# Optimization experiments

Hardware: AMD Instinct MI355X
Metric: run time of the kernel (lower is better)

## Reference

```python
import jax, jax.numpy as jnp
import numpy as np

B, L, D, H, TOPK = 64, 1024, 16, 128, 64
SCALE = H ** -0.5  # proj_dim ** -0.5


def _linear_params(k, fan_in, fan_out):
    W = jax.random.normal(k, (fan_in, fan_out), jnp.float32) / np.sqrt(fan_in).astype(np.float32)
    b = jnp.zeros((fan_out,), jnp.float32)
    return W, b


def setup_inputs() -> dict:
    key = jax.random.key(0)
    ks = jax.random.split(key, 9)
    x = jax.random.normal(ks[0], (B, L, D), jnp.float32)
    Wq, bq = _linear_params(ks[1], D, H)
    Wk, bk = _linear_params(ks[2], D, H)
    phi_W1, phi_b1 = _linear_params(ks[3], D, H)
    phi_W2, phi_b2 = _linear_params(ks[4], H, H)
    xi_W1, xi_b1 = _linear_params(ks[5], 2 * D, H)
    xi_W2, xi_b2 = _linear_params(ks[6], H, H)
    rho_W1, rho_b1 = _linear_params(ks[7], H, H)
    rho_W2, rho_b2 = _linear_params(ks[8], H, H)
    return {
        "x": x,
        "Wq": Wq, "bq": bq, "Wk": Wk, "bk": bk,
        "phi_W1": phi_W1, "phi_b1": phi_b1, "phi_W2": phi_W2, "phi_b2": phi_b2,
        "xi_W1": xi_W1, "xi_b1": xi_b1, "xi_W2": xi_W2, "xi_b2": xi_b2,
        "rho_W1": rho_W1, "rho_b1": rho_b1, "rho_W2": rho_W2, "rho_b2": rho_b2,
    }


def _gather_rows(x, idx):
    # x: (B, L, D), idx: (B, K) -> (B, K, D)
    return jnp.take_along_axis(x, jnp.broadcast_to(idx[:, :, None], idx.shape + (x.shape[-1],)), axis=1)


def reference(x, Wq, bq, Wk, bk,
              phi_W1, phi_b1, phi_W2, phi_b2,
              xi_W1, xi_b1, xi_W2, xi_b2,
              rho_W1, rho_b1, rho_W2, rho_b2):
    # padding mask (trim is identity for dense random inputs; mask is all-True)
    mask = jnp.abs(x).sum(-1) != 0  # (B, L)
    Q = x @ Wq + bq                 # (B, L, H)
    K = x @ Wk + bk                 # (B, L, H)
    scores = jnp.einsum("blh,bmh->blm", Q, K) * SCALE  # (B, L, L)
    mask_2d = mask[:, :, None] & mask[:, None, :]
    scores = jnp.where(mask_2d, scores, -jnp.inf)
    flat = scores.reshape(B, L * L)
    topk_vals, topk_idx = jax.lax.top_k(flat, TOPK)    # (B, K)
    topk_w = jax.nn.softmax(topk_vals, axis=-1)
    row = topk_idx // L
    col = topk_idx % L
    x_i = _gather_rows(x, row)  # (B, K, D)
    x_j = _gather_rows(x, col)
    relu = jax.nn.relu
    feat_self = relu(x_i @ phi_W1 + phi_b1) @ phi_W2 + phi_b2
    pair = jnp.concatenate([x_i, x_j], axis=-1)
    feat_pair = relu(pair @ xi_W1 + xi_b1) @ xi_W2 + xi_b2
    self_mask = (row == col)[:, :, None]
    interaction = jnp.where(self_mask, feat_self, feat_pair)  # (B, K, H)
    pooled = jnp.sum(interaction * topk_w[:, :, None], axis=1)  # (B, H)
    return relu(pooled @ rho_W1 + rho_b1) @ rho_W2 + rho_b2
```

## Files before the change

### kernel.cpp

```cpp
#include <hip/hip_runtime.h>

typedef unsigned int uint;

#define SCALEF 0.08838834764831845f
#define NBINS 4096
#define CAND_MAX 4096
#define SELC 1024
#define LLIST 512
#define T_LOOSE 3.3f

__device__ __forceinline__ uint ordmap(float v) {
  uint u = __float_as_uint(v);
  return (u & 0x80000000u) ? ~u : (u | 0x80000000u);
}

#define DOT4(a, b2) ((a).x*(b2).x + (a).y*(b2).y + (a).z*(b2).z + (a).w*(b2).w)

__global__ __launch_bounds__(256) void k_prep(const float* __restrict__ x,
    const float* __restrict__ Wq, const float* __restrict__ bq,
    const float* __restrict__ Wk, const float* __restrict__ bk,
    float* __restrict__ Gv, float* __restrict__ Hv,
    uint* __restrict__ ghist, uint* __restrict__ ccnt, uint* __restrict__ ccnt2) {
  __shared__ float sWq[2048], sWk[2048];
  __shared__ float sA[256];
  __shared__ float su[16], sv[16], sc;
  int tid = threadIdx.x;
  int row = blockIdx.x * 256 + tid;
  ((uint4*)ghist)[row] = make_uint4(0u, 0u, 0u, 0u);
  if (blockIdx.x == 0 && tid < 128) { if (tid < 64) ccnt[tid] = 0; else ccnt2[tid - 64] = 0; }
  for (int i = tid; i < 512; i += 256) {
    ((float4*)sWq)[i] = ((const float4*)Wq)[i];
    ((float4*)sWk)[i] = ((const float4*)Wk)[i];
  }
  __syncthreads();
  {
    int d = tid >> 4, e = tid & 15;
    float s = 0.f;
#pragma unroll 8
    for (int h = 0; h < 128; h++) s += sWq[d * 128 + h] * sWk[e * 128 + h];
    sA[tid] = s * SCALEF;
  }
  if (tid < 16) {
    float s1 = 0.f, s2 = 0.f;
    for (int h = 0; h < 128; h++) { s1 += sWq[tid * 128 + h] * bk[h]; s2 += bq[h] * sWk[tid * 128 + h]; }
    su[tid] = s1 * SCALEF; sv[tid] = s2 * SCALEF;
  } else if (tid == 16) {
    float s = 0.f;
    for (int h = 0; h < 128; h++) s += bq[h] * bk[h];
    sc = s * SCALEF;
  }
  __syncthreads();
  float xr[16];
#pragma unroll
  for (int d = 0; d < 16; d += 4) *(float4*)&xr[d] = *(const float4*)&x[(size_t)row * 16 + d];
  float g[16];
#pragma unroll
  for (int e = 0; e < 16; e++) {
    float s = sv[e];
#pragma unroll
    for (int d = 0; d < 16; d++) s += xr[d] * sA[d * 16 + e];
    g[e] = s;
  }
  float hh = sc;
#pragma unroll
  for (int d = 0; d < 16; d++) hh += xr[d] * su[d];
#pragma unroll
  for (int e = 0; e < 16; e += 4) *(float4*)&Gv[(size_t)row * 16 + e] = *(float4*)&g[e];
  Hv[row] = hh;
}

template<int PHASE>
__global__ __launch_bounds__(256, 4) void k_score(const float* __restrict__ Gv,
    const float* __restrict__ Hv, const float* __restrict__ x,
    uint* __restrict__ ghist, uint* __restrict__ ccnt,
    int* __restrict__ cidx, float* __restrict__ cval,
    const float* __restrict__ tcut2, const uint* __restrict__ ccmain) {
  int i = blockIdx.x;
  int b = i >> 6, t = i & 63, tm = t >> 3, tn = t & 7;
  if (PHASE != 0) { uint c = ccmain[b]; if (c >= 64 && c <= CAND_MAX) return; }
  __shared__ float4 sX4[512];
  __shared__ int lidx[PHASE == 1 ? 1 : LLIST];
  __shared__ float lval[PHASE == 1 ? 1 : LLIST];
  __shared__ uint lcnt, base_sh;
  __shared__ uint shist[PHASE == 1 ? NBINS : 1];
  int tid = threadIdx.x;
  if (PHASE == 1)
    for (int s = tid; s < NBINS; s += 256) shist[s] = 0;
  if (tid == 0) lcnt = 0;
  const float4* xsrc = (const float4*)(x + ((size_t)b * 1024 + tn * 128) * 16);
  sX4[tid] = xsrc[tid];
  sX4[tid + 256] = xsrc[tid + 256];
  int lane = tid & 63, w = tid >> 6;
  const float4* gp = (const float4*)(Gv + ((size_t)b * 1024 + tm * 128 + lane) * 16);
  float4 gr0[4], gr1[4];
#pragma unroll
  for (int q = 0; q < 4; q++) { gr0[q] = gp[q]; gr1[q] = gp[256 + q]; }
  float h0 = Hv[b * 1024 + tm * 128 + lane];
  float h1v = Hv[b * 1024 + tm * 128 + lane + 64];
  float tc = (PHASE == 2) ? tcut2[b] : T_LOOSE;
  int r0g = tm * 128 + lane, c0g = tn * 128;
  __syncthreads();

#pragma unroll 4
  for (int cc = 0; cc < 32; ++cc) {
    int c = w * 32 + cc;
    float4 x0 = sX4[c * 4 + 0], x1 = sX4[c * 4 + 1];
    float4 x2 = sX4[c * 4 + 2], x3 = sX4[c * 4 + 3];
    float s0 = (h0 + DOT4(gr0[0], x0) + DOT4(gr0[1], x1)) + (DOT4(gr0[2], x2) + DOT4(gr0[3], x3));
    float s1 = (h1v + DOT4(gr1[0], x0) + DOT4(gr1[1], x1)) + (DOT4(gr1[2], x2) + DOT4(gr1[3], x3));
    if (PHASE == 1) {
      atomicAdd(&shist[ordmap(s0) >> 20], 1u);
      atomicAdd(&shist[ordmap(s1) >> 20], 1u);
    } else {
      if (s0 >= tc) {
        uint pos = atomicAdd(&lcnt, 1u);
        int fi = r0g * 1024 + (c0g + c);
        if (pos < LLIST) { lidx[pos] = fi; lval[pos] = s0; }
        else { uint gp2 = atomicAdd(&ccnt[b], 1u);
               if (gp2 < CAND_MAX) { cidx[b * CAND_MAX + gp2] = fi; cval[b * CAND_MAX + gp2] = s0; } }
      }
      if (s1 >= tc) {
        uint pos = atomicAdd(&lcnt, 1u);
        int fi = (r0g + 64) * 1024 + (c0g + c);
        if (pos < LLIST) { lidx[pos] = fi; lval[pos] = s1; }
        else { uint gp2 = atomicAdd(&ccnt[b], 1u);
               if (gp2 < CAND_MAX) { cidx[b * CAND_MAX + gp2] = fi; cval[b * CAND_MAX + gp2] = s1; } }
      }
    }
  }
  __syncthreads();
  if (PHASE == 1) {
    for (int s = tid; s < NBINS; s += 256) { uint cg = shist[s]; if (cg) atomicAdd(&ghist[b * NBINS + s], cg); }
  } else {
    uint n = lcnt > LLIST ? LLIST : lcnt;
    if (tid == 0) base_sh = atomicAdd(&ccnt[b], n);
    __syncthreads();
    for (uint j = tid; j < n; j += 256) {
      uint p = base_sh + j;
      if (p < CAND_MAX) { cidx[b * CAND_MAX + p] = lidx[j]; cval[b * CAND_MAX + p] = lval[j]; }
    }
  }
}

__global__ __launch_bounds__(256) void k_fb_thresh(const uint* __restrict__ ghist,
    const uint* __restrict__ ccmain, float* __restrict__ tcut2) {
  int b = blockIdx.x;
  { uint c = ccmain[b]; if (c >= 64 && c <= CAND_MAX) return; }
  int tid = threadIdx.x;
  __shared__ uint hsh[NBINS];
  __shared__ uint csuf[256];
  __shared__ uint total_sh;
  for (int i = tid; i < NBINS; i += 256) hsh[i] = ghist[b * NBINS + i];
  __syncthreads();
  uint s = 0;
#pragma unroll
  for (int i = 0; i < 16; i++) s += hsh[tid * 16 + i];
  csuf[tid] = s;
  __syncthreads();
  if (tid == 0) {
    uint run = 0;
    for (int t2 = 255; t2 >= 0; t2--) { uint tmp = csuf[t2]; csuf[t2] = run; run += tmp; }
    total_sh = run;
  }
  __syncthreads();
  if (total_sh < 64) { if (tid == 0) tcut2[b] = -1e30f; return; }
  uint above = csuf[tid];
  if (above < 64) {
    uint run = above;
    for (int i = 15; i >= 0; i--) {
      run += hsh[tid * 16 + i];
      if (run >= 64) {
        uint umin = ((uint)(tid * 16 + i)) << 20;
        float lower = (umin & 0x80000000u) ? __uint_as_float(umin ^ 0x80000000u)
                                           : __uint_as_float(~umin);
        tcut2[b] = lower;
        break;
      }
    }
  }
}

__device__ __forceinline__ void suffix_find(const uint* __restrict__ h1,
    uint* __restrict__ wtot, int tid, uint K,
    uint* __restrict__ bin_out, uint* __restrict__ above_out) {
  int lane = tid & 63, w = tid >> 6;
  uint s = h1[tid * 4] + h1[tid * 4 + 1] + h1[tid * 4 + 2] + h1[tid * 4 + 3];
  uint acc = s;
#pragma unroll
  for (int off = 1; off < 64; off <<= 1) {
    uint o = __shfl_down(acc, off);
    if (lane + off < 64) acc += o;
  }
  if (lane == 0) wtot[w] = acc;
  __syncthreads();
  uint wsuf = 0;
#pragma unroll
  for (int ww = 0; ww < 16; ww++) if (ww > w) wsuf += wtot[ww];
  uint suf_incl = acc + wsuf;
  uint suf_excl = suf_incl - s;
  if (suf_excl < K && suf_incl >= K) {
    uint run = suf_excl;
    for (int i2 = 3; i2 >= 0; i2--) {
      uint hv = h1[tid * 4 + i2];
      run += hv;
      if (run >= K) { *bin_out = (uint)(tid * 4 + i2); *above_out = run - hv; break; }
    }
  }
  __syncthreads();
}

__global__ __launch_bounds__(1024) void k_final(const float* __restrict__ x,
    const float* __restrict__ phiW1, const float* __restrict__ phib1,
    const float* __restrict__ phiW2, const float* __restrict__ phib2,
    const float* __restrict__ xiW1, const float* __restrict__ xib1,
    const float* __restrict__ xiW2, const float* __restrict__ xib2,
    const float* __restrict__ rhoW1, const float* __restrict__ rhob1,
    const float* __restrict__ rhoW2, const float* __restrict__ rhob2,
    const uint* __restrict__ ccnt, const int* __restrict__ cidx, const float* __restrict__ cval,
    const uint* __restrict__ ccnt2, const int* __restrict__ cidx2, const float* __restrict__ cval2,
    float* __restrict__ out) {
  int b = blockIdx.x;
  int tid = threadIdx.x;
  __shared__ float svals[CAND_MAX];
  __shared__ int   sidxs[CAND_MAX];
  __shared__ uint  h1[NBINS];
  __shared__ uint  wtot[16];
  __shared__ uint  bin_sh, above_sh;
  __shared__ float cv[SELC];
  __shared__ int   ci[SELC];
  __shared__ int   scnt_sh;
  __shared__ float sel_v[64], sel_w[64];
  __shared__ int   sel_l[64], sel_m[64];
  __shared__ float xpair[2048];
  __shared__ float psv[8][128], ppv[8][128];
  __shared__ float hsv[128], hpv[128];
  __shared__ float pacc[8][128];
  __shared__ float vec1[128], vec2[128];
  __shared__ float wsums[2];

  uint cmain = ccnt[b];
  int fl = (cmain < 64 || cmain > CAND_MAX) ? 1 : 0;
  const int*   clist = fl ? (cidx2 + (size_t)b * CAND_MAX) : (cidx + (size_t)b * CAND_MAX);
  const float* vlist = fl ? (cval2 + (size_t)b * CAND_MAX) : (cval + (size_t)b * CAND_MAX);
  uint craw = fl ? ccnt2[b] : cmain;
  int cnt = craw > CAND_MAX ? CAND_MAX : (int)craw;

  for (int j = tid; j < cnt; j += 1024) { svals[j] = vlist[j]; sidxs[j] = clist[j]; }
  for (int s = tid; s < NBINS; s += 1024) h1[s] = 0;
  if (tid == 0) scnt_sh = 0;
  if (tid < 64) { sel_v[tid] = -1e30f; sel_l[tid] = 0; sel_m[tid] = 0; }
  __syncthreads();

  for (int j = tid; j < cnt; j += 1024) atomicAdd(&h1[ordmap(svals[j]) >> 20], 1u);
  __syncthreads();
  suffix_find(h1, wtot, tid, 64u, &bin_sh, &above_sh);
  uint B1 = bin_sh;
  uint need = 64u - above_sh;
  for (int s = tid; s < NBINS; s += 1024) h1[s] = 0;
  __syncthreads();
  for (int j = tid; j < cnt; j += 1024) {
    uint um = ordmap(svals[j]);
    if ((um >> 20) == B1) atomicAdd(&h1[(um >> 8) & 0xfffu], 1u);
  }
  __syncthreads();
  suffix_find(h1, wtot, tid, need, &bin_sh, &above_sh);
  uint P = (B1 << 12) | bin_sh;

  for (int j = tid; j < cnt; j += 1024) {
    uint um = ordmap(svals[j]);
    if ((um >> 8) >= P) {
      int pos = atomicAdd(&scnt_sh, 1);
      if (pos < SELC) { cv[pos] = svals[j]; ci[pos] = sidxs[j]; }
    }
  }
  __syncthreads();
  int S = scnt_sh < SELC ? scnt_sh : SELC;

  for (int j = tid; j < S; j += 1024) {
    float vj = cv[j]; int ij = ci[j];
    int rank = 0;
    for (int i2 = 0; i2 < S; i2++) {
      float vi = cv[i2]; int ii = ci[i2];
      rank += (vi > vj || (vi == vj && ii < ij)) ? 1 : 0;
    }
    if (rank < 64) { sel_v[rank] = vj; sel_l[rank] = ij >> 10; sel_m[rank] = ij & 1023; }
  }
  __syncthreads();

  if (tid < 64) {
    float e = expf(sel_v[tid] - sel_v[0]);
    float ssum = e;
#pragma unroll
    for (int off = 1; off < 64; off <<= 1) ssum += __shfl_xor(ssum, off);
    float wj = e / ssum;
    sel_w[tid] = wj;
    int isself = (sel_l[tid] == sel_m[tid]) ? 1 : 0;
    float s0 = isself ? wj : 0.f, s1 = isself ? 0.f : wj;
#pragma unroll
    for (int off = 1; off < 64; off <<= 1) { s0 += __shfl_xor(s0, off); s1 += __shfl_xor(s1, off); }
    if (tid == 0) { wsums[0] = s0; wsums[1] = s1; }
  } else if (tid >= 512) {
    int t2 = tid - 512;
    int j = t2 >> 3, q = t2 & 7;
    int r = (q < 4) ? sel_l[j] : sel_m[j];
    ((float4*)xpair)[j * 8 + q] = *(const float4*)&x[((size_t)b * 1024 + r) * 16 + (q & 3) * 4];
  }
  __syncthreads();

  {
    int slice = tid >> 7, h = tid & 127;
    float wphi[16], wxi[32];
#pragma unroll
    for (int d = 0; d < 16; d++) wphi[d] = phiW1[d * 128 + h];
#pragma unroll
    for (int d = 0; d < 32; d++) wxi[d] = xiW1[d * 128 + h];
    float bphi = phib1[h], bxi = xib1[h];
    float accphi = 0.f, accxi = 0.f;
#pragma unroll
    for (int jj = 0; jj < 8; jj++) {
      int j = slice * 8 + jj;
      int l = sel_l[j], m = sel_m[j];
      float wj = sel_w[j];
      if (l == m) {
        float a = bphi;
#pragma unroll
        for (int d = 0; d < 16; d++) a += xpair[j * 32 + d] * wphi[d];
        accphi += wj * fmaxf(a, 0.f);
      } else {
        float a = bxi;
#pragma unroll
        for (int d = 0; d < 32; d++) a += xpair[j * 32 + d] * wxi[d];
        accxi += wj * fmaxf(a, 0.f);
      }
    }
    psv[slice][h] = accphi;
    ppv[slice][h] = accxi;
  }
  __syncthreads();
  if (tid < 256) {
    int hh = tid & 127;
    float s = 0.f;
    if (tid < 128) {
#pragma unroll
      for (int s2 = 0; s2 < 8; s2++) s += psv[s2][hh];
      hsv[hh] = s;
    } else {
#pragma unroll
      for (int s2 = 0; s2 < 8; s2++) s += ppv[s2][hh];
      hpv[hh] = s;
    }
  }
  __syncthreads();

  {
    int sl = tid >> 7, o = tid & 127;
    float p = 0.f;
#pragma unroll
    for (int hh2 = 0; hh2 < 16; hh2++) {
      int hh = sl * 16 + hh2;
      p += hsv[hh] * phiW2[hh * 128 + o] + hpv[hh] * xiW2[hh * 128 + o];
    }
    pacc[sl][o] = p;
  }
  __syncthreads();
  if (tid < 128) {
    float p = wsums[0] * phib2[tid] + wsums[1] * xib2[tid];
#pragma unroll
    for (int s2 = 0; s2 < 8; s2++) p += pacc[s2][tid];
    vec1[tid] = p;
  }
  __syncthreads();
  {
    int sl = tid >> 7, o = tid & 127;
    float p = 0.f;
#pragma unroll
    for (int hh2 = 0; hh2 < 16; hh2++) {
      int hh = sl * 16 + hh2;
      p += vec1[hh] * rhoW1[hh * 128 + o];
    }
    pacc[sl][o] = p;
  }
  __syncthreads();
  if (tid < 128) {
    float r = rhob1[tid];
#pragma unroll
    for (int s2 = 0; s2 < 8; s2++) r += pacc[s2][tid];
    vec2[tid] = fmaxf(r, 0.f);
  }
  __syncthreads();
  {
    int sl = tid >> 7, o = tid & 127;
    float p = 0.f;
#pragma unroll
    for (int hh2 = 0; hh2 < 16; hh2++) {
      int hh = sl * 16 + hh2;
      p += vec2[hh] * rhoW2[hh * 128 + o];
    }
    pacc[sl][o] = p;
  }
  __syncthreads();
  if (tid < 128) {
    float o2 = rhob2[tid];
#pragma unroll
    for (int s2 = 0; s2 < 8; s2++) o2 += pacc[s2][tid];
    out[(size_t)b * 128 + tid] = o2;
  }
}

extern "C" void kernel_launch(void* const* d_in, const int* in_sizes, int n_in,
                              void* d_out, int out_size, void* d_ws, size_t ws_size,
                              hipStream_t stream) {
  (void)in_sizes; (void)n_in; (void)out_size; (void)ws_size;
  const float* x     = (const float*)d_in[0];
  const float* Wq    = (const float*)d_in[1];
  const float* bq    = (const float*)d_in[2];
  const float* Wk    = (const float*)d_in[3];
  const float* bk    = (const float*)d_in[4];
  const float* phiW1 = (const float*)d_in[5];
  const float* phib1 = (const float*)d_in[6];
  const float* phiW2 = (const float*)d_in[7];
  const float* phib2 = (const float*)d_in[8];
  const float* xiW1  = (const float*)d_in[9];
  const float* xib1  = (const float*)d_in[10];
  const float* xiW2  = (const float*)d_in[11];
  const float* xib2  = (const float*)d_in[12];
  const float* rhoW1 = (const float*)d_in[13];
  const float* rhob1 = (const float*)d_in[14];
  const float* rhoW2 = (const float*)d_in[15];
  const float* rhob2 = (const float*)d_in[16];

  char* ws = (char*)d_ws;
  float* Gv   = (float*)(ws);
  float* Hv   = (float*)(ws + 4194304);
  uint*  ghist= (uint*)(ws + 4456448);
  uint*  ccnt = (uint*)(ws + 5505024);
  uint*  ccnt2= (uint*)(ws + 5505280);
  float* tcut2= (float*)(ws + 5505536);
  int*   cidx = (int*)(ws + 5506304);
  float* cval = (float*)(ws + 6554880);
  int*   cidx2= (int*)(ws + 7603456);
  float* cval2= (float*)(ws + 8652032);

  k_prep<<<256, 256, 0, stream>>>(x, Wq, bq, Wk, bk, Gv, Hv, ghist, ccnt, ccnt2);
  k_score<0><<<4096, 256, 0, stream>>>(Gv, Hv, x, nullptr, ccnt, cidx, cval, nullptr, nullptr);
  k_score<1><<<4096, 256, 0, stream>>>(Gv, Hv, x, ghist, nullptr, nullptr, nullptr, nullptr, ccnt);
  k_fb_thresh<<<64, 256, 0, stream>>>(ghist, ccnt, tcut2);
  k_score<2><<<4096, 256, 0, stream>>>(Gv, Hv, x, nullptr, ccnt2, cidx2, cval2, tcut2, ccnt);
  k_final<<<64, 1024, 0, stream>>>(x,
                                  phiW1, phib1, phiW2, phib2,
                                  xiW1, xib1, xiW2, xib2,
                                  rhoW1, rhob1, rhoW2, rhob2,
                                  ccnt, cidx, cval, ccnt2, cidx2, cval2,
                                  (float*)d_out);
}
```

Baseline: 172.5 us.

## Replace three-pass histogram fallback with single per-batch radix-select kernel; widen score tiles

The fallback path (histogram pass, threshold kernel, rescoring pass) is replaced by one k_fallback kernel per batch that recomputes scores in-block and does a two-level radix select. The two extra full-grid k_score launches and the ghist zeroing go away, so the common path pays only for early-exit blocks. The main score kernel now computes four rows per thread instead of two, which halves the grid and reuses each shared-memory x load across more rows. The cost is higher register pressure in k_score and a slow serial fallback whenever it actually triggers.

```diff
diff --git a/kernel.cpp b/kernel.cpp
--- a/kernel.cpp
+++ b/kernel.cpp
@@ -1,6 +1,7 @@
 #include <hip/hip_runtime.h>
 
 typedef unsigned int uint;
+typedef __attribute__((ext_vector_type(4))) float f4;
 
 #define SCALEF 0.08838834764831845f
 #define NBINS 4096
@@ -20,13 +21,12 @@
     const float* __restrict__ Wq, const float* __restrict__ bq,
     const float* __restrict__ Wk, const float* __restrict__ bk,
     float* __restrict__ Gv, float* __restrict__ Hv,
-    uint* __restrict__ ghist, uint* __restrict__ ccnt, uint* __restrict__ ccnt2) {
+    uint* __restrict__ ccnt, uint* __restrict__ ccnt2) {
   __shared__ float sWq[2048], sWk[2048];
   __shared__ float sA[256];
   __shared__ float su[16], sv[16], sc;
   int tid = threadIdx.x;
   int row = blockIdx.x * 256 + tid;
-  ((uint4*)ghist)[row] = make_uint4(0u, 0u, 0u, 0u);
   if (blockIdx.x == 0 && tid < 128) { if (tid < 64) ccnt[tid] = 0; else ccnt2[tid - 64] = 0; }
   for (int i = tid; i < 512; i += 256) {
     ((float4*)sWq)[i] = ((const float4*)Wq)[i];
@@ -69,114 +69,65 @@
   Hv[row] = hh;
 }
 
-template<int PHASE>
 __global__ __launch_bounds__(256, 4) void k_score(const float* __restrict__ Gv,
     const float* __restrict__ Hv, const float* __restrict__ x,
-    uint* __restrict__ ghist, uint* __restrict__ ccnt,
-    int* __restrict__ cidx, float* __restrict__ cval,
-    const float* __restrict__ tcut2, const uint* __restrict__ ccmain) {
+    uint* __restrict__ ccnt, int* __restrict__ cidx, float* __restrict__ cval) {
   int i = blockIdx.x;
-  int b = i >> 6, t = i & 63, tm = t >> 3, tn = t & 7;
-  if (PHASE != 0) { uint c = ccmain[b]; if (c >= 64 && c <= CAND_MAX) return; }
-  __shared__ float4 sX4[512];
-  __shared__ int lidx[PHASE == 1 ? 1 : LLIST];
-  __shared__ float lval[PHASE == 1 ? 1 : LLIST];
+  int b = i >> 5, t = i & 31, tm = t >> 3, tn = t & 7;
+  __shared__ f4 sX4[512];
+  __shared__ int lidx[LLIST];
+  __shared__ float lval[LLIST];
   __shared__ uint lcnt, base_sh;
-  __shared__ uint shist[PHASE == 1 ? NBINS : 1];
   int tid = threadIdx.x;
-  if (PHASE == 1)
-    for (int s = tid; s < NBINS; s += 256) shist[s] = 0;
   if (tid == 0) lcnt = 0;
-  const float4* xsrc = (const float4*)(x + ((size_t)b * 1024 + tn * 128) * 16);
+  const f4* xsrc = (const f4*)(x + ((size_t)b * 1024 + tn * 128) * 16);
   sX4[tid] = xsrc[tid];
   sX4[tid + 256] = xsrc[tid + 256];
   int lane = tid & 63, w = tid >> 6;
-  const float4* gp = (const float4*)(Gv + ((size_t)b * 1024 + tm * 128 + lane) * 16);
-  float4 gr0[4], gr1[4];
-#pragma unroll
-  for (int q = 0; q < 4; q++) { gr0[q] = gp[q]; gr1[q] = gp[256 + q]; }
-  float h0 = Hv[b * 1024 + tm * 128 + lane];
-  float h1v = Hv[b * 1024 + tm * 128 + lane + 64];
-  float tc = (PHASE == 2) ? tcut2[b] : T_LOOSE;
-  int r0g = tm * 128 + lane, c0g = tn * 128;
-  __syncthreads();
-
-#pragma unroll 4
+  const f4* gp = (const f4*)(Gv + ((size_t)b * 1024 + tm * 256 + lane) * 16);
+  f4 gr[4][4];
+  float hv[4];
+#pragma unroll
+  for (int k = 0; k < 4; k++) {
+#pragma unroll
+    for (int q = 0; q < 4; q++) gr[k][q] = gp[k * 256 + q];
+    hv[k] = Hv[b * 1024 + tm * 256 + lane + 64 * k];
+  }
+  asm volatile("" : "+v"(gr[0][0]), "+v"(gr[0][1]), "+v"(gr[0][2]), "+v"(gr[0][3]),
+                    "+v"(gr[1][0]), "+v"(gr[1][1]), "+v"(gr[1][2]), "+v"(gr[1][3]));
+  asm volatile("" : "+v"(gr[2][0]), "+v"(gr[2][1]), "+v"(gr[2][2]), "+v"(gr[2][3]),
+                    "+v"(gr[3][0]), "+v"(gr[3][1]), "+v"(gr[3][2]), "+v"(gr[3][3]));
+  int r0g = tm * 256 + lane, c0g = tn * 128;
+  __syncthreads();
+
+#pragma unroll 2
   for (int cc = 0; cc < 32; ++cc) {
     int c = w * 32 + cc;
-    float4 x0 = sX4[c * 4 + 0], x1 = sX4[c * 4 + 1];
-    float4 x2 = sX4[c * 4 + 2], x3 = sX4[c * 4 + 3];
-    float s0 = (h0 + DOT4(gr0[0], x0) + DOT4(gr0[1], x1)) + (DOT4(gr0[2], x2) + DOT4(gr0[3], x3));
-    float s1 = (h1v + DOT4(gr1[0], x0) + DOT4(gr1[1], x1)) + (DOT4(gr1[2], x2) + DOT4(gr1[3], x3));
-    if (PHASE == 1) {
-      atomicAdd(&shist[ordmap(s0) >> 20], 1u);
-      atomicAdd(&shist[ordmap(s1) >> 20], 1u);
-    } else {
-      if (s0 >= tc) {
+    f4 x0 = sX4[c * 4 + 0], x1 = sX4[c * 4 + 1];
+    f4 x2 = sX4[c * 4 + 2], x3 = sX4[c * 4 + 3];
+    float s[4];
+#pragma unroll
+    for (int k = 0; k < 4; k++)
+      s[k] = (hv[k] + DOT4(gr[k][0], x0) + DOT4(gr[k][1], x1))
+           + (DOT4(gr[k][2], x2) + DOT4(gr[k][3], x3));
+#pragma unroll
+    for (int k = 0; k < 4; k++) {
+      if (__builtin_expect(s[k] >= T_LOOSE, 0)) {
         uint pos = atomicAdd(&lcnt, 1u);
-        int fi = r0g * 1024 + (c0g + c);
-        if (pos < LLIST) { lidx[pos] = fi; lval[pos] = s0; }
+        int fi = (r0g + 64 * k) * 1024 + (c0g + c);
+        if (pos < LLIST) { lidx[pos] = fi; lval[pos] = s[k]; }
         else { uint gp2 = atomicAdd(&ccnt[b], 1u);
-               if (gp2 < CAND_MAX) { cidx[b * CAND_MAX + gp2] = fi; cval[b * CAND_MAX + gp2] = s0; } }
+               if (gp2 < CAND_MAX) { cidx[b * CAND_MAX + gp2] = fi; cval[b * CAND_MAX + gp2] = s[k]; } }
       }
-      if (s1 >= tc) {
-        uint pos = atomicAdd(&lcnt, 1u);
-        int fi = (r0g + 64) * 1024 + (c0g + c);
-        if (pos < LLIST) { lidx[pos] = fi; lval[pos] = s1; }
-        else { uint gp2 = atomicAdd(&ccnt[b], 1u);
-               if (gp2 < CAND_MAX) { cidx[b * CAND_MAX + gp2] = fi; cval[b * CAND_MAX + gp2] = s1; } }
-      }
-    }
-  }
-  __syncthreads();
-  if (PHASE == 1) {
-    for (int s = tid; s < NBINS; s += 256) { uint cg = shist[s]; if (cg) atomicAdd(&ghist[b * NBINS + s], cg); }
-  } else {
-    uint n = lcnt > LLIST ? LLIST : lcnt;
-    if (tid == 0) base_sh = atomicAdd(&ccnt[b], n);
-    __syncthreads();
-    for (uint j = tid; j < n; j += 256) {
-      uint p = base_sh + j;
-      if (p < CAND_MAX) { cidx[b * CAND_MAX + p] = lidx[j]; cval[b * CAND_MAX + p] = lval[j]; }
-    }
-  }
-}
-
-__global__ __launch_bounds__(256) void k_fb_thresh(const uint* __restrict__ ghist,
-    const uint* __restrict__ ccmain, float* __restrict__ tcut2) {
-  int b = blockIdx.x;
-  { uint c = ccmain[b]; if (c >= 64 && c <= CAND_MAX) return; }
-  int tid = threadIdx.x;
-  __shared__ uint hsh[NBINS];
-  __shared__ uint csuf[256];
-  __shared__ uint total_sh;
-  for (int i = tid; i < NBINS; i += 256) hsh[i] = ghist[b * NBINS + i];
-  __syncthreads();
-  uint s = 0;
-#pragma unroll
-  for (int i = 0; i < 16; i++) s += hsh[tid * 16 + i];
-  csuf[tid] = s;
-  __syncthreads();
-  if (tid == 0) {
-    uint run = 0;
-    for (int t2 = 255; t2 >= 0; t2--) { uint tmp = csuf[t2]; csuf[t2] = run; run += tmp; }
-    total_sh = run;
-  }
-  __syncthreads();
-  if (total_sh < 64) { if (tid == 0) tcut2[b] = -1e30f; return; }
-  uint above = csuf[tid];
-  if (above < 64) {
-    uint run = above;
-    for (int i = 15; i >= 0; i--) {
-      run += hsh[tid * 16 + i];
-      if (run >= 64) {
-        uint umin = ((uint)(tid * 16 + i)) << 20;
-        float lower = (umin & 0x80000000u) ? __uint_as_float(umin ^ 0x80000000u)
-                                           : __uint_as_float(~umin);
-        tcut2[b] = lower;
-        break;
-      }
-    }
+    }
+  }
+  __syncthreads();
+  uint n = lcnt > LLIST ? LLIST : lcnt;
+  if (tid == 0) base_sh = atomicAdd(&ccnt[b], n);
+  __syncthreads();
+  for (uint j = tid; j < n; j += 256) {
+    uint p = base_sh + j;
+    if (p < CAND_MAX) { cidx[b * CAND_MAX + p] = lidx[j]; cval[b * CAND_MAX + p] = lval[j]; }
   }
 }
 
@@ -207,6 +158,58 @@
     }
   }
   __syncthreads();
+}
+
+__global__ __launch_bounds__(1024) void k_fallback(const float* __restrict__ Gv,
+    const float* __restrict__ Hv, const float* __restrict__ x,
+    const uint* __restrict__ ccnt, uint* __restrict__ ccnt2,
+    int* __restrict__ cidx2, float* __restrict__ cval2) {
+  int b = blockIdx.x;
+  { uint c = ccnt[b]; if (c >= 64 && c <= CAND_MAX) return; }
+  __shared__ uint h1[NBINS];
+  __shared__ uint wtot[16];
+  __shared__ uint bin_sh, above_sh;
+  int tid = threadIdx.x;
+  float xm[16];
+#pragma unroll
+  for (int d = 0; d < 16; d += 4) *(float4*)&xm[d] = *(const float4*)&x[((size_t)b * 1024 + tid) * 16 + d];
+  for (int s2 = tid; s2 < NBINS; s2 += 1024) h1[s2] = 0;
+  __syncthreads();
+  for (int l = 0; l < 1024; l++) {
+    float s = Hv[b * 1024 + l];
+    const float* gl = Gv + ((size_t)b * 1024 + l) * 16;
+#pragma unroll
+    for (int d = 0; d < 16; d++) s += gl[d] * xm[d];
+    atomicAdd(&h1[ordmap(s) >> 20], 1u);
+  }
+  __syncthreads();
+  suffix_find(h1, wtot, tid, 64u, &bin_sh, &above_sh);
+  uint B1 = bin_sh;
+  uint need = 64u - above_sh;
+  for (int s2 = tid; s2 < NBINS; s2 += 1024) h1[s2] = 0;
+  __syncthreads();
+  for (int l = 0; l < 1024; l++) {
+    float s = Hv[b * 1024 + l];
+    const float* gl = Gv + ((size_t)b * 1024 + l) * 16;
+#pragma unroll
+    for (int d = 0; d < 16; d++) s += gl[d] * xm[d];
+    uint um = ordmap(s);
+    if ((um >> 20) == B1) atomicAdd(&h1[(um >> 8) & 0xfffu], 1u);
+  }
+  __syncthreads();
+  suffix_find(h1, wtot, tid, need, &bin_sh, &above_sh);
+  uint P = (B1 << 12) | bin_sh;
+  for (int l = 0; l < 1024; l++) {
+    float s = Hv[b * 1024 + l];
+    const float* gl = Gv + ((size_t)b * 1024 + l) * 16;
+#pragma unroll
+    for (int d = 0; d < 16; d++) s += gl[d] * xm[d];
+    uint um = ordmap(s);
+    if ((um >> 8) >= P) {
+      uint pos = atomicAdd(&ccnt2[b], 1u);
+      if (pos < CAND_MAX) { cidx2[b * CAND_MAX + pos] = l * 1024 + tid; cval2[b * CAND_MAX + pos] = s; }
+    }
+  }
 }
 
 __global__ __launch_bounds__(1024) void k_final(const float* __restrict__ x,
@@ -432,20 +435,16 @@
   char* ws = (char*)d_ws;
   float* Gv   = (float*)(ws);
   float* Hv   = (float*)(ws + 4194304);
-  uint*  ghist= (uint*)(ws + 4456448);
-  uint*  ccnt = (uint*)(ws + 5505024);
-  uint*  ccnt2= (uint*)(ws + 5505280);
-  float* tcut2= (float*)(ws + 5505536);
-  int*   cidx = (int*)(ws + 5506304);
-  float* cval = (float*)(ws + 6554880);
-  int*   cidx2= (int*)(ws + 7603456);
-  float* cval2= (float*)(ws + 8652032);
-
-  k_prep<<<256, 256, 0, stream>>>(x, Wq, bq, Wk, bk, Gv, Hv, ghist, ccnt, ccnt2);
-  k_score<0><<<4096, 256, 0, stream>>>(Gv, Hv, x, nullptr, ccnt, cidx, cval, nullptr, nullptr);
-  k_score<1><<<4096, 256, 0, stream>>>(Gv, Hv, x, ghist, nullptr, nullptr, nullptr, nullptr, ccnt);
-  k_fb_thresh<<<64, 256, 0, stream>>>(ghist, ccnt, tcut2);
-  k_score<2><<<4096, 256, 0, stream>>>(Gv, Hv, x, nullptr, ccnt2, cidx2, cval2, tcut2, ccnt);
+  uint*  ccnt = (uint*)(ws + 4456448);
+  uint*  ccnt2= (uint*)(ws + 4456704);
+  int*   cidx = (int*)(ws + 4457472);
+  float* cval = (float*)(ws + 5506048);
+  int*   cidx2= (int*)(ws + 6554624);
+  float* cval2= (float*)(ws + 7603200);
+
+  k_prep<<<256, 256, 0, stream>>>(x, Wq, bq, Wk, bk, Gv, Hv, ccnt, ccnt2);
+  k_score<<<2048, 256, 0, stream>>>(Gv, Hv, x, ccnt, cidx, cval);
+  k_fallback<<<64, 1024, 0, stream>>>(Gv, Hv, x, ccnt, ccnt2, cidx2, cval2);
   k_final<<<64, 1024, 0, stream>>>(x,
                                   phiW1, phib1, phiW2, phib2,
                                   xiW1, xib1, xiW2, xib2,
```

New measurement: 162.5 us. -5.8%, faster.
